# Kernel tuning notes

Hardware: AMD Instinct MI355X
Metric: run time of the kernel (lower is better)

Reference implementation:

```python
import jax, jax.numpy as jnp
import numpy as np

N_NODES = 50000
N_EDGES = 500000
MUL0, MUL1 = 16, 8          # multiplicities of 0e and 1o irreps (in == out)
DIM = MUL0 + 3 * MUL1       # 40
N_BASIS, MID = 10, 32
WNUM = MUL0*MUL0 + MUL1*MUL0 + MUL0*MUL1 + MUL1*MUL1  # 576
INV_SQRT3 = 1.0 / np.sqrt(3.0)  # wigner-3j normalization for l=1 paths
FAN_IN = MUL0 + MUL1        # paths into each output irrep: 16 + 8 = 24
A0 = np.sqrt(1.0 / FAN_IN)  # sqrt((2*0+1)/fan_in)
A1 = np.sqrt(3.0 / FAN_IN)  # sqrt((2*1+1)/fan_in)
LN_EPS = 1e-5


def setup_inputs() -> dict:
    key = jax.random.key(0)
    ks = jax.random.split(key, 8)
    return {
        "x": jax.random.normal(ks[0], (N_NODES, DIM), jnp.float32),
        "edge_sh": jax.random.normal(ks[1], (N_EDGES, 4), jnp.float32),
        "edge_length_embedded": jax.random.uniform(ks[2], (N_EDGES, N_BASIS), jnp.float32),
        "W1": jax.random.normal(ks[3], (N_BASIS, MID), jnp.float32),
        "W2": jax.random.normal(ks[4], (MID, WNUM), jnp.float32),
        "gamma": jnp.ones((DIM,), jnp.float32),
        "beta": jnp.zeros((DIM,), jnp.float32),
        "edge_src": jax.random.randint(ks[5], (N_EDGES,), 0, N_NODES),
        "edge_dst": jax.random.randint(ks[6], (N_EDGES,), 0, N_NODES),
        "avg_num_neighbors": 10,
    }


def reference(x, edge_sh, edge_length_embedded, W1, W2, gamma, beta,
              edge_src, edge_dst, avg_num_neighbors):
    # radial MLP -> per-edge tensor-product weights (e3nn FullyConnectedNet style)
    h = jax.nn.silu(edge_length_embedded @ W1 / jnp.sqrt(jnp.float32(N_BASIS)))
    w = h @ W2 / jnp.sqrt(jnp.float32(MID))              # [E, 576]

    # gather node features onto edges and split into irrep blocks
    xg = x[edge_src]                                     # [E, 40]
    s = xg[:, :MUL0]                                     # [E, 16]  scalars 0e
    v = xg[:, MUL0:].reshape(-1, MUL1, 3)                # [E, 8, 3] vectors 1o
    sh0 = edge_sh[:, 0]                                  # [E]
    sh1 = edge_sh[:, 1:4]                                # [E, 3]

    # split per-edge weights by tensor-product path
    o0, o1, o2 = MUL0*MUL0, MUL0*MUL0 + MUL1*MUL0, MUL0*MUL0 + MUL1*MUL0 + MUL0*MUL1
    W_ss0 = w[:, :o0].reshape(-1, MUL0, MUL0)            # 0e x 0e -> 0e
    W_vv0 = w[:, o0:o1].reshape(-1, MUL1, MUL0)          # 1o x 1o -> 0e
    W_sv1 = w[:, o1:o2].reshape(-1, MUL0, MUL1)          # 0e x 1o -> 1o
    W_vs1 = w[:, o2:].reshape(-1, MUL1, MUL1)            # 1o x 0e -> 1o

    # weighted Clebsch-Gordan tensor product (per edge)
    vdot = jnp.einsum('eui,ei->eu', v, sh1) * INV_SQRT3  # CG 1x1->0
    out0 = A0 * (jnp.einsum('euk,eu->ek', W_ss0, s * sh0[:, None])
                 + jnp.einsum('euk,eu->ek', W_vv0, vdot))            # [E, 16]
    out1 = A1 * INV_SQRT3 * (
        jnp.einsum('euk,eu->ek', W_sv1, s)[:, :, None] * sh1[:, None, :]
        + jnp.einsum('euk,eui->eki', W_vs1, v) * sh0[:, None, None])  # [E, 8, 3]
    edge_values = jnp.concatenate([out0, out1.reshape(-1, 3 * MUL1)], axis=1)

    # scatter-sum into destination nodes, degree normalization, layernorm
    node = jax.ops.segment_sum(edge_values, edge_dst, num_segments=N_NODES)
    node = node / jnp.sqrt(jnp.float32(avg_num_neighbors))
    mu = node.mean(axis=-1, keepdims=True)
    var = node.var(axis=-1, keepdims=True)
    return (node - mu) * jax.lax.rsqrt(var + LN_EPS) * gamma + beta
```

## Files before the change

kernel.cpp:

```cpp
#include <hip/hip_runtime.h>
#include <hip/hip_bf16.h>

#define N_NODES 50000
#define N_EDGES 500000
#define MUL0 16
#define MUL1 8
#define DIM 40
#define N_BASIS 10
#define MID 32
#define WNUM 576
#define SCAN_BLOCKS 196
#define N_GROUPS (N_EDGES / 16)

typedef __attribute__((ext_vector_type(8))) short bf16x8_t;
typedef __attribute__((ext_vector_type(4))) float f32x4_t;

__device__ __forceinline__ float bf2f(unsigned short u) {
  return __uint_as_float(((unsigned int)u) << 16);
}
__device__ __forceinline__ unsigned short f2bf(float f) {
  unsigned int x = __float_as_uint(f);
  unsigned int r = x + 0x7fffu + ((x >> 16) & 1u);
  return (unsigned short)(r >> 16);
}
__device__ __forceinline__ unsigned pk2bf(float a, float b) {
  float2 f; f.x = a; f.y = b;
  __hip_bfloat162 h = __float22bfloat162_rn(f);
  return *reinterpret_cast<unsigned*>(&h);
}
__device__ __forceinline__ bool detect_bf16(const void* gamma) {
  return ((const unsigned int*)gamma)[0] == 0x3F803F80u;
}
template <bool BF16>
__device__ __forceinline__ float ld(const void* p, size_t i) {
  if (BF16) return bf2f(((const unsigned short*)p)[i]);
  return ((const float*)p)[i];
}

#define C_INV_SQRT10 0.31622776601683794f
#define C_INV_SQRT32 0.17677669529663687f
#define C_INV_SQRT3  0.5773502691896258f
#define C_A0C        0.20412414523193154f

__device__ __forceinline__ f32x4_t mfma16x16x32(bf16x8_t a, bf16x8_t b, f32x4_t c) {
  return __builtin_amdgcn_mfma_f32_16x16x32_bf16(a, b, c, 0, 0, 0);
}

__device__ __forceinline__ void gload4(const float* g, float* l) {
  __builtin_amdgcn_global_load_lds(
      (const __attribute__((address_space(1))) void*)g,
      (__attribute__((address_space(3))) void*)l, 4, 0, 0);
}

__global__ __launch_bounds__(256) void rank_kernel(
    const int* __restrict__ edge_dst, int* __restrict__ cnt,
    int* __restrict__ rank) {
  int e = blockIdx.x * 256 + threadIdx.x;
  if (e < N_EDGES) rank[e] = atomicAdd(&cnt[edge_dst[e]], 1);
}

__global__ __launch_bounds__(256) void scanA_kernel(
    const int* __restrict__ cnt, int* __restrict__ off, int* __restrict__ btot) {
  __shared__ int s[256];
  const int tid = threadIdx.x;
  const int i = blockIdx.x * 256 + tid;
  int v = (i < N_NODES) ? cnt[i] : 0;
  s[tid] = v;
  __syncthreads();
  for (int d = 1; d < 256; d <<= 1) {
    int t = (tid >= d) ? s[tid - d] : 0;
    __syncthreads();
    s[tid] += t;
    __syncthreads();
  }
  if (i < N_NODES) off[i] = s[tid] - v;
  if (tid == 255) btot[blockIdx.x] = s[255];
}

__global__ __launch_bounds__(256) void scanB_kernel(
    const int* __restrict__ btot, int* __restrict__ off) {
  __shared__ int s[256];
  __shared__ int basev;
  const int tid = threadIdx.x;
  int v = (tid < SCAN_BLOCKS) ? btot[tid] : 0;
  s[tid] = v;
  __syncthreads();
  for (int d = 1; d < 256; d <<= 1) {
    int t = (tid >= d) ? s[tid - d] : 0;
    __syncthreads();
    s[tid] += t;
    __syncthreads();
  }
  if (tid == 0) basev = (blockIdx.x == 0) ? 0 : s[blockIdx.x - 1];
  __syncthreads();
  const int i = blockIdx.x * 256 + tid;
  if (i < N_NODES) off[i] += basev;
}


#define STAGE_OPS 11

__device__ __forceinline__ void stage_issue(float* Sn, int g, int psrc,
                                            const float* xf, const float* shf,
                                            int lane) {
  const int quad = lane >> 4;
  const int l16  = lane & 15;
  gload4(shf + ((size_t)g * 16 + l16) * 4 + quad, Sn);
  const float* gx = xf + (size_t)psrc * DIM + quad;
  #pragma unroll
  for (int i = 0; i < 10; ++i) {
    float* lb = (i < 4) ? (Sn + 64 + 64 * i) : (Sn + 192 + 64 * i);
    gload4(gx + i * 4, lb);
  }
}

template <bool BF16>
__device__ void edge_mfma_body(
    const void* __restrict__ x,
    const void* __restrict__ edge_sh,
    const void* __restrict__ elemb,
    const void* __restrict__ W1,
    const void* __restrict__ W2,
    const int* __restrict__ edge_src,
    const int* __restrict__ edge_dst,
    const int* __restrict__ rank,
    const int* __restrict__ off,
    unsigned short* __restrict__ ev,
    short* __restrict__ w2b, float* __restrict__ w1s, float* __restrict__ stg)
{
  const int tid = threadIdx.x;

  for (int i = tid; i < 36 * 512; i += 256) {
    int m = i / WNUM;
    int col = i - m * WNUM;
    int q = m >> 3, j = m & 7;
    int t = col >> 4, n = col & 15;
    short val;
    if (BF16) val = (short)((const unsigned short*)W2)[i];
    else      val = (short)f2bf(((const float*)W2)[i]);
    w2b[t * 512 + q * 128 + n * 8 + j] = val;
  }
  for (int i = tid; i < N_BASIS * MID; i += 256) w1s[i] = ld<BF16>(W1, i);
  __syncthreads();

  const int lane = tid & 63;
  const int wid  = tid >> 6;
  const int quad = lane >> 4;
  const int l16  = lane & 15;
  float* Sw = stg + wid * 1664;

  if constexpr (BF16) {
    float* S = Sw;
    for (int gi = blockIdx.x * 4 + wid; gi < N_GROUPS; gi += gridDim.x * 4) {
      const int e0 = gi * 16;
      __builtin_amdgcn_wave_barrier();
      const int eL   = e0 + l16;
      const int dL   = edge_dst[eL];
      const int posv = off[dL] + rank[eL];
      const int posA = __shfl(posv, lane >> 2, 64);
      const int posB = posv;
      if (lane < 16) {
        uint2 sw = *reinterpret_cast<const uint2*>(
            (const unsigned short*)edge_sh + (size_t)(e0 + lane) * 4);
        S[0 * 16 + lane] = __uint_as_float(sw.x << 16);
        S[1 * 16 + lane] = __uint_as_float(sw.x & 0xffff0000u);
        S[2 * 16 + lane] = __uint_as_float(sw.y << 16);
        S[3 * 16 + lane] = __uint_as_float(sw.y & 0xffff0000u);
      }
      {
        const int src = edge_src[e0 + l16];
        const uint4* xr = reinterpret_cast<const uint4*>(
            (const unsigned short*)x + (size_t)src * DIM);
        uint4 c = xr[quad];
        unsigned wv[4] = {c.x, c.y, c.z, c.w};
        #pragma unroll
        for (int p = 0; p < 4; ++p) {
          int col = quad * 8 + 2 * p;
          float lo = __uint_as_float(wv[p] << 16);
          float hi = __uint_as_float(wv[p] & 0xffff0000u);
          int off0 = (col < 16) ? (64 + col * 16) : (448 + (col - 16) * 16);
          int off1 = (col + 1 < 16) ? (64 + (col + 1) * 16) : (448 + (col - 15) * 16);
          S[off0 + l16] = lo;
          S[off1 + l16] = hi;
        }
        if (lane < 16) {
          uint4 c4 = xr[4];
          unsigned wv4[4] = {c4.x, c4.y, c4.z, c4.w};
          #pragma unroll
          for (int p = 0; p < 4; ++p) {
            int col = 32 + 2 * p;
            S[448 + (col - 16) * 16 + lane] = __uint_as_float(wv4[p] << 16);
            S[448 + (col - 15) * 16 + lane] = __uint_as_float(wv4[p] & 0xffff0000u);
          }
        }
      }
      __builtin_amdgcn_wave_barrier();
      #pragma unroll
      for (int p = 0; p < 2; ++p) {
        int idx = lane + p * 64;
        int u = idx >> 4, e = idx & 15;
        float vdv = (S[448 + (u * 3 + 0) * 16 + e] * S[16 + e] +
                     S[448 + (u * 3 + 1) * 16 + e] * S[32 + e] +
                     S[448 + (u * 3 + 2) * 16 + e] * S[48 + e]) * C_INV_SQRT3;
        S[320 + u * 16 + e] = vdv;
      }
      __builtin_amdgcn_wave_barrier();
      bf16x8_t af;
      {
        float eb[N_BASIS];
        const unsigned short* er = (const unsigned short*)elemb + (size_t)(e0 + l16) * N_BASIS;
        #pragma unroll
        for (int p = 0; p < 5; ++p) {
          unsigned uv = *reinterpret_cast<const unsigned*>(er + p * 2);
          eb[2 * p]     = __uint_as_float(uv << 16);
          eb[2 * p + 1] = __uint_as_float(uv & 0xffff0000u);
        }
        float hv[8];
        #pragma unroll
        for (int j = 0; j < 8; ++j) {
          int k = quad * 8 + j;
          float p = 0.f;
          #pragma unroll
          for (int b = 0; b < N_BASIS; ++b) p += eb[b] * w1s[b * MID + k];
          float z = p * C_INV_SQRT10;
          hv[j] = z / (1.f + __expf(-z)) * C_INV_SQRT32;
        }
        __align__(16) unsigned au[4];
        #pragma unroll
        for (int j = 0; j < 4; ++j) au[j] = pk2bf(hv[2 * j], hv[2 * j + 1]);
        af = *reinterpret_cast<const bf16x8_t*>(au);
      }
      f32x4_t s0 = *reinterpret_cast<const f32x4_t*>(&S[quad * 4]);
      f32x4_t out0 = {0.f,0.f,0.f,0.f}, tsv = {0.f,0.f,0.f,0.f};
      f32x4_t tv0 = {0.f,0.f,0.f,0.f}, tv1 = {0.f,0.f,0.f,0.f}, tv2 = {0.f,0.f,0.f,0.f};
      const f32x4_t zero = {0.f,0.f,0.f,0.f};
      const int usel = (l16 >> 3);
      #pragma unroll
      for (int t = 0; t < 16; ++t) {
        bf16x8_t bf = *reinterpret_cast<const bf16x8_t*>(&w2b[t * 512 + lane * 8]);
        f32x4_t D = mfma16x16x32(af, bf, zero);
        f32x4_t sv = *reinterpret_cast<const f32x4_t*>(&S[64 + t * 16 + quad * 4]);
        out0 += D * (sv * s0);
      }
      #pragma unroll
      for (int t = 0; t < 8; ++t) {
        bf16x8_t bf = *reinterpret_cast<const bf16x8_t*>(&w2b[(16 + t) * 512 + lane * 8]);
        f32x4_t D = mfma16x16x32(af, bf, zero);
        f32x4_t vdv = *reinterpret_cast<const f32x4_t*>(&S[320 + t * 16 + quad * 4]);
        out0 += D * vdv;
      }
      #pragma unroll
      for (int t = 0; t < 8; ++t) {
        bf16x8_t bf = *reinterpret_cast<const bf16x8_t*>(&w2b[(24 + t) * 512 + lane * 8]);
        f32x4_t D = mfma16x16x32(af, bf, zero);
        int u = 2 * t + usel;
        f32x4_t sv = *reinterpret_cast<const f32x4_t*>(&S[64 + u * 16 + quad * 4]);
        tsv += D * sv;
      }
      #pragma unroll
      for (int t = 0; t < 4; ++t) {
        bf16x8_t bf = *reinterpret_cast<const bf16x8_t*>(&w2b[(32 + t) * 512 + lane * 8]);
        f32x4_t D = mfma16x16x32(af, bf, zero);
        int u = 2 * t + usel;
        f32x4_t v0 = *reinterpret_cast<const f32x4_t*>(&S[448 + (u * 3 + 0) * 16 + quad * 4]);
        f32x4_t v1 = *reinterpret_cast<const f32x4_t*>(&S[448 + (u * 3 + 1) * 16 + quad * 4]);
        f32x4_t v2 = *reinterpret_cast<const f32x4_t*>(&S[448 + (u * 3 + 2) * 16 + quad * 4]);
        tv0 += D * v0; tv1 += D * v1; tv2 += D * v2;
      }
      #pragma unroll
      for (int r = 0; r < 4; ++r) {
        tsv[r] += __shfl_xor(tsv[r], 8, 64);
        tv0[r] += __shfl_xor(tv0[r], 8, 64);
        tv1[r] += __shfl_xor(tv1[r], 8, 64);
        tv2[r] += __shfl_xor(tv2[r], 8, 64);
      }
      __builtin_amdgcn_wave_barrier();
      #pragma unroll
      for (int r = 0; r < 4; ++r)
        S[64 + (quad * 4 + r) * 42 + l16] = C_A0C * out0[r];
      if (l16 < 8) {
        f32x4_t h1x = *reinterpret_cast<const f32x4_t*>(&S[16 + quad * 4]);
        f32x4_t h1y = *reinterpret_cast<const f32x4_t*>(&S[32 + quad * 4]);
        f32x4_t h1z = *reinterpret_cast<const f32x4_t*>(&S[48 + quad * 4]);
        #pragma unroll
        for (int r = 0; r < 4; ++r) {
          int rowb = 64 + (quad * 4 + r) * 42 + 16 + 3 * l16;
          S[rowb + 0] = C_A0C * (tsv[r] * h1x[r] + tv0[r] * s0[r]);
          S[rowb + 1] = C_A0C * (tsv[r] * h1y[r] + tv1[r] * s0[r]);
          S[rowb + 2] = C_A0C * (tsv[r] * h1z[r] + tv2[r] * s0[r]);
        }
      }
      __builtin_amdgcn_wave_barrier();
      {
        const int edge = lane >> 2, chunk = lane & 3;
        const float* rp = &S[64 + edge * 42 + chunk * 8];
        uint4 t;
        t.x = pk2bf(rp[0], rp[1]); t.y = pk2bf(rp[2], rp[3]);
        t.z = pk2bf(rp[4], rp[5]); t.w = pk2bf(rp[6], rp[7]);
        *reinterpret_cast<uint4*>(ev + (size_t)posA * DIM + chunk * 8) = t;
        if (lane < 16) {
          const float* rq = &S[64 + lane * 42 + 32];
          uint4 t2;
          t2.x = pk2bf(rq[0], rq[1]); t2.y = pk2bf(rq[2], rq[3]);
          t2.z = pk2bf(rq[4], rq[5]); t2.w = pk2bf(rq[6], rq[7]);
          *reinterpret_cast<uint4*>(ev + (size_t)posB * DIM + 32) = t2;
        }
      }
    }
    return;
  }

  const float* xf  = (const float*)x;
  const float* shf = (const float*)edge_sh;
  const int stride = gridDim.x * 4;
  const int gi0 = blockIdx.x * 4 + wid;

  int pdst, psrc, prank;
  int cdst, crank;
  {
    const int e = gi0 * 16 + l16;
    pdst = edge_dst[e]; psrc = edge_src[e]; prank = rank[e];
  }
  stage_issue(Sw, gi0, psrc, xf, shf, lane);
  cdst = pdst; crank = prank;
  {
    const int g1 = gi0 + stride;
    if (g1 < N_GROUPS) {
      const int e = g1 * 16 + l16;
      pdst = edge_dst[e]; psrc = edge_src[e]; prank = rank[e];
    }
  }

  int cur = 0;
  for (int gi = gi0; gi < N_GROUPS; gi += stride, cur ^= 1) {
    float* S  = Sw + cur * 832;
    float* Sn = Sw + (cur ^ 1) * 832;
    const int e0 = gi * 16;
    const int g1 = gi + stride;

    __builtin_amdgcn_wave_barrier();
    if (g1 < N_GROUPS) {
      stage_issue(Sn, g1, psrc, xf, shf, lane);
      asm volatile("s_waitcnt vmcnt(11)" ::: "memory");
    } else {
      asm volatile("s_waitcnt vmcnt(0)" ::: "memory");
    }
    __builtin_amdgcn_sched_barrier(0);

    const int ndst = pdst, nrank = prank;
    {
      const int g2 = g1 + stride;
      if (g2 < N_GROUPS) {
        const int e = g2 * 16 + l16;
        pdst = edge_dst[e]; psrc = edge_src[e]; prank = rank[e];
      }
    }
    const int posv = off[cdst] + crank;
    const int posA = __shfl(posv, lane >> 2, 64);
    const int posB = posv;

    #pragma unroll
    for (int p = 0; p < 2; ++p) {
      int idx = lane + p * 64;
      int u = idx >> 4, e = idx & 15;
      float vdv = (S[448 + (u * 3 + 0) * 16 + e] * S[16 + e] +
                   S[448 + (u * 3 + 1) * 16 + e] * S[32 + e] +
                   S[448 + (u * 3 + 2) * 16 + e] * S[48 + e]) * C_INV_SQRT3;
      S[320 + u * 16 + e] = vdv;
    }
    __builtin_amdgcn_wave_barrier();

    bf16x8_t af;
    {
      float eb[N_BASIS];
      const float* er = (const float*)elemb + (size_t)(e0 + l16) * N_BASIS;
      #pragma unroll
      for (int p = 0; p < 5; ++p) {
        float2 fv = *reinterpret_cast<const float2*>(er + p * 2);
        eb[2 * p] = fv.x; eb[2 * p + 1] = fv.y;
      }
      float hv[8];
      #pragma unroll
      for (int j = 0; j < 8; ++j) {
        int k = quad * 8 + j;
        float p = 0.f;
        #pragma unroll
        for (int b = 0; b < N_BASIS; ++b) p += eb[b] * w1s[b * MID + k];
        float z = p * C_INV_SQRT10;
        hv[j] = z / (1.f + __expf(-z)) * C_INV_SQRT32;
      }
      __align__(16) unsigned au[4];
      #pragma unroll
      for (int j = 0; j < 4; ++j) au[j] = pk2bf(hv[2 * j], hv[2 * j + 1]);
      af = *reinterpret_cast<const bf16x8_t*>(au);
    }

    f32x4_t s0 = *reinterpret_cast<const f32x4_t*>(&S[quad * 4]);

    f32x4_t out0 = {0.f, 0.f, 0.f, 0.f};
    f32x4_t tsv  = {0.f, 0.f, 0.f, 0.f};
    f32x4_t tv0  = {0.f, 0.f, 0.f, 0.f};
    f32x4_t tv1  = {0.f, 0.f, 0.f, 0.f};
    f32x4_t tv2  = {0.f, 0.f, 0.f, 0.f};
    const f32x4_t zero = {0.f, 0.f, 0.f, 0.f};
    const int usel = (l16 >> 3);

    #pragma unroll
    for (int t = 0; t < 16; ++t) {
      bf16x8_t bf = *reinterpret_cast<const bf16x8_t*>(&w2b[t * 512 + lane * 8]);
      f32x4_t D = mfma16x16x32(af, bf, zero);
      f32x4_t sv = *reinterpret_cast<const f32x4_t*>(&S[64 + t * 16 + quad * 4]);
      out0 += D * (sv * s0);
    }
    #pragma unroll
    for (int t = 0; t < 8; ++t) {
      bf16x8_t bf = *reinterpret_cast<const bf16x8_t*>(&w2b[(16 + t) * 512 + lane * 8]);
      f32x4_t D = mfma16x16x32(af, bf, zero);
      f32x4_t vdv = *reinterpret_cast<const f32x4_t*>(&S[320 + t * 16 + quad * 4]);
      out0 += D * vdv;
    }
    #pragma unroll
    for (int t = 0; t < 8; ++t) {
      bf16x8_t bf = *reinterpret_cast<const bf16x8_t*>(&w2b[(24 + t) * 512 + lane * 8]);
      f32x4_t D = mfma16x16x32(af, bf, zero);
      int u = 2 * t + usel;
      f32x4_t sv = *reinterpret_cast<const f32x4_t*>(&S[64 + u * 16 + quad * 4]);
      tsv += D * sv;
    }
    #pragma unroll
    for (int t = 0; t < 4; ++t) {
      bf16x8_t bf = *reinterpret_cast<const bf16x8_t*>(&w2b[(32 + t) * 512 + lane * 8]);
      f32x4_t D = mfma16x16x32(af, bf, zero);
      int u = 2 * t + usel;
      f32x4_t v0 = *reinterpret_cast<const f32x4_t*>(&S[448 + (u * 3 + 0) * 16 + quad * 4]);
      f32x4_t v1 = *reinterpret_cast<const f32x4_t*>(&S[448 + (u * 3 + 1) * 16 + quad * 4]);
      f32x4_t v2 = *reinterpret_cast<const f32x4_t*>(&S[448 + (u * 3 + 2) * 16 + quad * 4]);
      tv0 += D * v0; tv1 += D * v1; tv2 += D * v2;
    }

    #pragma unroll
    for (int r = 0; r < 4; ++r) {
      tsv[r] += __shfl_xor(tsv[r], 8, 64);
      tv0[r] += __shfl_xor(tv0[r], 8, 64);
      tv1[r] += __shfl_xor(tv1[r], 8, 64);
      tv2[r] += __shfl_xor(tv2[r], 8, 64);
    }
    __builtin_amdgcn_wave_barrier();

    #pragma unroll
    for (int r = 0; r < 4; ++r)
      S[64 + (quad * 4 + r) * 42 + l16] = C_A0C * out0[r];
    if (l16 < 8) {
      f32x4_t h1x = *reinterpret_cast<const f32x4_t*>(&S[16 + quad * 4]);
      f32x4_t h1y = *reinterpret_cast<const f32x4_t*>(&S[32 + quad * 4]);
      f32x4_t h1z = *reinterpret_cast<const f32x4_t*>(&S[48 + quad * 4]);
      #pragma unroll
      for (int r = 0; r < 4; ++r) {
        int rowb = 64 + (quad * 4 + r) * 42 + 16 + 3 * l16;
        S[rowb + 0] = C_A0C * (tsv[r] * h1x[r] + tv0[r] * s0[r]);
        S[rowb + 1] = C_A0C * (tsv[r] * h1y[r] + tv1[r] * s0[r]);
        S[rowb + 2] = C_A0C * (tsv[r] * h1z[r] + tv2[r] * s0[r]);
      }
    }
    __builtin_amdgcn_wave_barrier();

    {
      const int edge = lane >> 2, chunk = lane & 3;
      const float* rp = &S[64 + edge * 42 + chunk * 8];
      uint4 t;
      t.x = pk2bf(rp[0], rp[1]); t.y = pk2bf(rp[2], rp[3]);
      t.z = pk2bf(rp[4], rp[5]); t.w = pk2bf(rp[6], rp[7]);
      *reinterpret_cast<uint4*>(ev + (size_t)posA * DIM + chunk * 8) = t;
      if (lane < 16) {
        const float* rq = &S[64 + lane * 42 + 32];
        uint4 t2;
        t2.x = pk2bf(rq[0], rq[1]); t2.y = pk2bf(rq[2], rq[3]);
        t2.z = pk2bf(rq[4], rq[5]); t2.w = pk2bf(rq[6], rq[7]);
        *reinterpret_cast<uint4*>(ev + (size_t)posB * DIM + 32) = t2;
      }
    }

    cdst = ndst; crank = nrank;
  }
}

__global__ __launch_bounds__(256, 2) void edge_mfma_kernel(
    const void* __restrict__ x,
    const void* __restrict__ edge_sh,
    const void* __restrict__ elemb,
    const void* __restrict__ W1,
    const void* __restrict__ W2,
    const void* __restrict__ gamma,
    const int* __restrict__ edge_src,
    const int* __restrict__ edge_dst,
    const int* __restrict__ rank,
    const int* __restrict__ off,
    unsigned short* __restrict__ ev)
{
  __shared__ __align__(16) short w2b[36 * 512];
  __shared__ __align__(16) float w1s[N_BASIS * MID];
  __shared__ __align__(16) float stg[4 * 1664];

  if (detect_bf16(gamma))
    edge_mfma_body<true >(x, edge_sh, elemb, W1, W2, edge_src, edge_dst, rank,
                          off, ev, w2b, w1s, stg);
  else
    edge_mfma_body<false>(x, edge_sh, elemb, W1, W2, edge_src, edge_dst, rank,
                          off, ev, w2b, w1s, stg);
}


#define NPW 12

template <bool BF16>
__device__ __forceinline__ void node_body(
    const unsigned short* __restrict__ ev,
    const int* __restrict__ cnt,
    const int* __restrict__ off,
    const void* __restrict__ gamma,
    const void* __restrict__ beta,
    const int* __restrict__ avg,
    void* __restrict__ out, int lane, int wv)
{
  const int slot = lane / 5;
  const int q    = lane - slot * 5;
  const int base = lane - q;
  const int n    = wv * NPW + slot;
  const bool valid = (slot < NPW) && (n < N_NODES);

  float s[8];
  #pragma unroll
  for (int d = 0; d < 8; ++d) s[d] = 0.f;

  int c = 0, o = 0;
  if (valid) { c = cnt[n]; o = off[n]; }

  const uint4* p = reinterpret_cast<const uint4*>(ev) + (size_t)o * 5 + q;
  int j = 0;
  for (; j + 1 < c; j += 2) {
    uint4 w0 = p[(size_t)j * 5];
    uint4 w1 = p[(size_t)(j + 1) * 5];
    unsigned a0[4] = {w0.x, w0.y, w0.z, w0.w};
    unsigned a1[4] = {w1.x, w1.y, w1.z, w1.w};
    #pragma unroll
    for (int k = 0; k < 4; ++k) {
      s[2 * k + 0] += __uint_as_float(a0[k] << 16) + __uint_as_float(a1[k] << 16);
      s[2 * k + 1] += __uint_as_float(a0[k] & 0xffff0000u) +
                      __uint_as_float(a1[k] & 0xffff0000u);
    }
  }
  if (j < c) {
    uint4 w0 = p[(size_t)j * 5];
    unsigned a0[4] = {w0.x, w0.y, w0.z, w0.w};
    #pragma unroll
    for (int k = 0; k < 4; ++k) {
      s[2 * k + 0] += __uint_as_float(a0[k] << 16);
      s[2 * k + 1] += __uint_as_float(a0[k] & 0xffff0000u);
    }
  }

  const float inv = rsqrtf((float)avg[0]);
  float psum = 0.f;
  #pragma unroll
  for (int d = 0; d < 8; ++d) { s[d] *= inv; psum += s[d]; }
  float m = 0.f;
  #pragma unroll
  for (int i = 0; i < 5; ++i) m += __shfl(psum, base + i, 64);
  const float mean = m * (1.f / DIM);
  float pvar = 0.f;
  #pragma unroll
  for (int d = 0; d < 8; ++d) { float dd = s[d] - mean; pvar += dd * dd; }
  float vv = 0.f;
  #pragma unroll
  for (int i = 0; i < 5; ++i) vv += __shfl(pvar, base + i, 64);
  const float var = vv * (1.f / DIM);
  const float r = rsqrtf(var + 1e-5f);

  if (!valid) return;
  const int gb = q * 8;
  if (BF16) {
    const uint4 g4 = reinterpret_cast<const uint4*>(gamma)[q];
    const uint4 b4 = reinterpret_cast<const uint4*>(beta)[q];
    unsigned gw[4] = {g4.x, g4.y, g4.z, g4.w};
    unsigned bw[4] = {b4.x, b4.y, b4.z, b4.w};
    uint4 t;
    unsigned tw[4];
    #pragma unroll
    for (int k = 0; k < 4; ++k) {
      float y0 = (s[2*k+0] - mean) * r * __uint_as_float(gw[k] << 16) +
                 __uint_as_float(bw[k] << 16);
      float y1 = (s[2*k+1] - mean) * r * __uint_as_float(gw[k] & 0xffff0000u) +
                 __uint_as_float(bw[k] & 0xffff0000u);
      tw[k] = pk2bf(y0, y1);
    }
    t.x = tw[0]; t.y = tw[1]; t.z = tw[2]; t.w = tw[3];
    *reinterpret_cast<uint4*>((unsigned short*)out + (size_t)n * DIM + gb) = t;
  } else {
    const float4 g0 = reinterpret_cast<const float4*>(gamma)[q * 2];
    const float4 g1 = reinterpret_cast<const float4*>(gamma)[q * 2 + 1];
    const float4 b0 = reinterpret_cast<const float4*>(beta)[q * 2];
    const float4 b1 = reinterpret_cast<const float4*>(beta)[q * 2 + 1];
    float4* op = reinterpret_cast<float4*>((float*)out + (size_t)n * DIM + gb);
    float4 t0, t1;
    t0.x = (s[0] - mean) * r * g0.x + b0.x;
    t0.y = (s[1] - mean) * r * g0.y + b0.y;
    t0.z = (s[2] - mean) * r * g0.z + b0.z;
    t0.w = (s[3] - mean) * r * g0.w + b0.w;
    t1.x = (s[4] - mean) * r * g1.x + b1.x;
    t1.y = (s[5] - mean) * r * g1.y + b1.y;
    t1.z = (s[6] - mean) * r * g1.z + b1.z;
    t1.w = (s[7] - mean) * r * g1.w + b1.w;
    op[0] = t0; op[1] = t1;
  }
}

__global__ __launch_bounds__(256) void node_kernel(
    const unsigned short* __restrict__ ev,
    const int* __restrict__ cnt,
    const int* __restrict__ off,
    const void* __restrict__ gamma,
    const void* __restrict__ beta,
    const int* __restrict__ avg,
    void* __restrict__ out)
{
  const int lane = threadIdx.x & 63;
  const int wv = blockIdx.x * 4 + (threadIdx.x >> 6);
  if (detect_bf16(gamma)) node_body<true >(ev, cnt, off, gamma, beta, avg, out, lane, wv);
  else                    node_body<false>(ev, cnt, off, gamma, beta, avg, out, lane, wv);
}

extern "C" void kernel_launch(void* const* d_in, const int* in_sizes, int n_in,
                              void* d_out, int out_size, void* d_ws, size_t ws_size,
                              hipStream_t stream) {
  const void* x       = d_in[0];
  const void* edge_sh = d_in[1];
  const void* elemb   = d_in[2];
  const void* W1      = d_in[3];
  const void* W2      = d_in[4];
  const void* gamma   = d_in[5];
  const void* beta    = d_in[6];
  const int* edge_src = (const int*)d_in[7];
  const int* edge_dst = (const int*)d_in[8];
  const int* avg      = (const int*)d_in[9];

  char* wsb = (char*)d_ws;
  unsigned short* ev = (unsigned short*)(wsb);
  int* rank  = (int*)(wsb + 40000000);
  int* cnt   = (int*)(wsb + 42000000);
  int* off   = (int*)(wsb + 42200000);
  int* btot  = (int*)(wsb + 42400000);

  hipMemsetAsync(cnt, 0, 200000, stream);

  const int EB = (N_EDGES + 255) / 256;
  rank_kernel <<<EB, 256, 0, stream>>>(edge_dst, cnt, rank);
  scanA_kernel<<<SCAN_BLOCKS, 256, 0, stream>>>(cnt, off, btot);
  scanB_kernel<<<SCAN_BLOCKS, 256, 0, stream>>>(btot, off);

  edge_mfma_kernel<<<512, 256, 0, stream>>>(x, edge_sh, elemb, W1, W2, gamma,
                                            edge_src, edge_dst, rank, off, ev);

  node_kernel<<<(N_NODES + 4 * NPW - 1) / (4 * NPW), 256, 0, stream>>>(
      ev, cnt, off, gamma, beta, avg, d_out);
}
```

Measured before the change: 209.8 us.

## Keep W2 MFMA B-fragments in registers instead of LDS, vectorize radial MLP

Each lane now loads its 36 bf16x8 W2 fragments directly from global memory into registers once per block. The 36 KB LDS staging copy of W2 is removed, along with the per-iteration LDS reads that fed the MFMAs. The first radial MLP layer is also restructured to use vector LDS reads of W1 rows with accumulate-over-basis. This adds 144 VGPRs per lane, which risks spilling or lower occupancy under the launch bound of 2 blocks. The vmcnt wait threshold is adjusted to match the changed number of outstanding loads.

```diff
diff --git a/kernel.cpp b/kernel.cpp
--- a/kernel.cpp
+++ b/kernel.cpp
@@ -98,8 +98,6 @@
 }
 
 
-#define STAGE_OPS 11
-
 __device__ __forceinline__ void stage_issue(float* Sn, int g, int psrc,
                                             const float* xf, const float* shf,
                                             int lane) {
@@ -111,6 +109,38 @@
   for (int i = 0; i < 10; ++i) {
     float* lb = (i < 4) ? (Sn + 64 + 64 * i) : (Sn + 192 + 64 * i);
     gload4(gx + i * 4, lb);
+  }
+}
+
+template <bool BF16>
+__device__ __forceinline__ void load_wb(const void* W2, int quad, int l16,
+                                        bf16x8_t* wb) {
+  if constexpr (BF16) {
+    const unsigned short* wcol = (const unsigned short*)W2 +
+                                 (size_t)(quad * 8) * WNUM + l16;
+    #pragma unroll
+    for (int t = 0; t < 36; ++t) {
+      __align__(16) unsigned au[4];
+      #pragma unroll
+      for (int jp = 0; jp < 4; ++jp) {
+        unsigned lo = wcol[(size_t)(2 * jp) * WNUM + 16 * t];
+        unsigned hi = wcol[(size_t)(2 * jp + 1) * WNUM + 16 * t];
+        au[jp] = lo | (hi << 16);
+      }
+      wb[t] = *reinterpret_cast<const bf16x8_t*>(au);
+    }
+  } else {
+    const float* wcol = (const float*)W2 + (size_t)(quad * 8) * WNUM + l16;
+    #pragma unroll
+    for (int t = 0; t < 36; ++t) {
+      __align__(16) unsigned au[4];
+      #pragma unroll
+      for (int jp = 0; jp < 4; ++jp) {
+        au[jp] = pk2bf(wcol[(size_t)(2 * jp) * WNUM + 16 * t],
+                       wcol[(size_t)(2 * jp + 1) * WNUM + 16 * t]);
+      }
+      wb[t] = *reinterpret_cast<const bf16x8_t*>(au);
+    }
   }
 }
 
@@ -126,28 +156,20 @@
     const int* __restrict__ rank,
     const int* __restrict__ off,
     unsigned short* __restrict__ ev,
-    short* __restrict__ w2b, float* __restrict__ w1s, float* __restrict__ stg)
+    float* __restrict__ w1s, float* __restrict__ stg)
 {
   const int tid = threadIdx.x;
-
-  for (int i = tid; i < 36 * 512; i += 256) {
-    int m = i / WNUM;
-    int col = i - m * WNUM;
-    int q = m >> 3, j = m & 7;
-    int t = col >> 4, n = col & 15;
-    short val;
-    if (BF16) val = (short)((const unsigned short*)W2)[i];
-    else      val = (short)f2bf(((const float*)W2)[i]);
-    w2b[t * 512 + q * 128 + n * 8 + j] = val;
-  }
   for (int i = tid; i < N_BASIS * MID; i += 256) w1s[i] = ld<BF16>(W1, i);
-  __syncthreads();
 
   const int lane = tid & 63;
   const int wid  = tid >> 6;
   const int quad = lane >> 4;
   const int l16  = lane & 15;
   float* Sw = stg + wid * 1664;
+
+  bf16x8_t wb[36];
+  load_wb<BF16>(W2, quad, l16, wb);
+  __syncthreads();
 
   if constexpr (BF16) {
     float* S = Sw;
@@ -217,12 +239,18 @@
         }
         float hv[8];
         #pragma unroll
+        for (int j = 0; j < 8; ++j) hv[j] = 0.f;
+        #pragma unroll
+        for (int b = 0; b < N_BASIS; ++b) {
+          const float e = eb[b];
+          f32x4_t wA = *reinterpret_cast<const f32x4_t*>(&w1s[b * MID + quad * 8]);
+          f32x4_t wB = *reinterpret_cast<const f32x4_t*>(&w1s[b * MID + quad * 8 + 4]);
+          hv[0] += e * wA[0]; hv[1] += e * wA[1]; hv[2] += e * wA[2]; hv[3] += e * wA[3];
+          hv[4] += e * wB[0]; hv[5] += e * wB[1]; hv[6] += e * wB[2]; hv[7] += e * wB[3];
+        }
+        #pragma unroll
         for (int j = 0; j < 8; ++j) {
-          int k = quad * 8 + j;
-          float p = 0.f;
-          #pragma unroll
-          for (int b = 0; b < N_BASIS; ++b) p += eb[b] * w1s[b * MID + k];
-          float z = p * C_INV_SQRT10;
+          float z = hv[j] * C_INV_SQRT10;
           hv[j] = z / (1.f + __expf(-z)) * C_INV_SQRT32;
         }
         __align__(16) unsigned au[4];
@@ -237,30 +265,26 @@
       const int usel = (l16 >> 3);
       #pragma unroll
       for (int t = 0; t < 16; ++t) {
-        bf16x8_t bf = *reinterpret_cast<const bf16x8_t*>(&w2b[t * 512 + lane * 8]);
-        f32x4_t D = mfma16x16x32(af, bf, zero);
+        f32x4_t D = mfma16x16x32(af, wb[t], zero);
         f32x4_t sv = *reinterpret_cast<const f32x4_t*>(&S[64 + t * 16 + quad * 4]);
         out0 += D * (sv * s0);
       }
       #pragma unroll
       for (int t = 0; t < 8; ++t) {
-        bf16x8_t bf = *reinterpret_cast<const bf16x8_t*>(&w2b[(16 + t) * 512 + lane * 8]);
-        f32x4_t D = mfma16x16x32(af, bf, zero);
+        f32x4_t D = mfma16x16x32(af, wb[16 + t], zero);
         f32x4_t vdv = *reinterpret_cast<const f32x4_t*>(&S[320 + t * 16 + quad * 4]);
         out0 += D * vdv;
       }
       #pragma unroll
       for (int t = 0; t < 8; ++t) {
-        bf16x8_t bf = *reinterpret_cast<const bf16x8_t*>(&w2b[(24 + t) * 512 + lane * 8]);
-        f32x4_t D = mfma16x16x32(af, bf, zero);
+        f32x4_t D = mfma16x16x32(af, wb[24 + t], zero);
         int u = 2 * t + usel;
         f32x4_t sv = *reinterpret_cast<const f32x4_t*>(&S[64 + u * 16 + quad * 4]);
         tsv += D * sv;
       }
       #pragma unroll
       for (int t = 0; t < 4; ++t) {
-        bf16x8_t bf = *reinterpret_cast<const bf16x8_t*>(&w2b[(32 + t) * 512 + lane * 8]);
-        f32x4_t D = mfma16x16x32(af, bf, zero);
+        f32x4_t D = mfma16x16x32(af, wb[32 + t], zero);
         int u = 2 * t + usel;
         f32x4_t v0 = *reinterpret_cast<const f32x4_t*>(&S[448 + (u * 3 + 0) * 16 + quad * 4]);
         f32x4_t v1 = *reinterpret_cast<const f32x4_t*>(&S[448 + (u * 3 + 1) * 16 + quad * 4]);
@@ -341,7 +365,7 @@
     __builtin_amdgcn_wave_barrier();
     if (g1 < N_GROUPS) {
       stage_issue(Sn, g1, psrc, xf, shf, lane);
-      asm volatile("s_waitcnt vmcnt(11)" ::: "memory");
+      asm volatile("s_waitcnt vmcnt(16)" ::: "memory");
     } else {
       asm volatile("s_waitcnt vmcnt(0)" ::: "memory");
     }
@@ -381,12 +405,18 @@
       }
       float hv[8];
       #pragma unroll
+      for (int j = 0; j < 8; ++j) hv[j] = 0.f;
+      #pragma unroll
+      for (int b = 0; b < N_BASIS; ++b) {
+        const float e = eb[b];
+        f32x4_t wA = *reinterpret_cast<const f32x4_t*>(&w1s[b * MID + quad * 8]);
+        f32x4_t wB = *reinterpret_cast<const f32x4_t*>(&w1s[b * MID + quad * 8 + 4]);
+        hv[0] += e * wA[0]; hv[1] += e * wA[1]; hv[2] += e * wA[2]; hv[3] += e * wA[3];
+        hv[4] += e * wB[0]; hv[5] += e * wB[1]; hv[6] += e * wB[2]; hv[7] += e * wB[3];
+      }
+      #pragma unroll
       for (int j = 0; j < 8; ++j) {
-        int k = quad * 8 + j;
-        float p = 0.f;
-        #pragma unroll
-        for (int b = 0; b < N_BASIS; ++b) p += eb[b] * w1s[b * MID + k];
-        float z = p * C_INV_SQRT10;
+        float z = hv[j] * C_INV_SQRT10;
         hv[j] = z / (1.f + __expf(-z)) * C_INV_SQRT32;
       }
       __align__(16) unsigned au[4];
@@ -407,30 +437,26 @@
 
     #pragma unroll
     for (int t = 0; t < 16; ++t) {
-      bf16x8_t bf = *reinterpret_cast<const bf16x8_t*>(&w2b[t * 512 + lane * 8]);
-      f32x4_t D = mfma16x16x32(af, bf, zero);
+      f32x4_t D = mfma16x16x32(af, wb[t], zero);
       f32x4_t sv = *reinterpret_cast<const f32x4_t*>(&S[64 + t * 16 + quad * 4]);
       out0 += D * (sv * s0);
     }
     #pragma unroll
     for (int t = 0; t < 8; ++t) {
-      bf16x8_t bf = *reinterpret_cast<const bf16x8_t*>(&w2b[(16 + t) * 512 + lane * 8]);
-      f32x4_t D = mfma16x16x32(af, bf, zero);
+      f32x4_t D = mfma16x16x32(af, wb[16 + t], zero);
       f32x4_t vdv = *reinterpret_cast<const f32x4_t*>(&S[320 + t * 16 + quad * 4]);
       out0 += D * vdv;
     }
     #pragma unroll
     for (int t = 0; t < 8; ++t) {
-      bf16x8_t bf = *reinterpret_cast<const bf16x8_t*>(&w2b[(24 + t) * 512 + lane * 8]);
-      f32x4_t D = mfma16x16x32(af, bf, zero);
+      f32x4_t D = mfma16x16x32(af, wb[24 + t], zero);
       int u = 2 * t + usel;
       f32x4_t sv = *reinterpret_cast<const f32x4_t*>(&S[64 + u * 16 + quad * 4]);
       tsv += D * sv;
     }
     #pragma unroll
     for (int t = 0; t < 4; ++t) {
-      bf16x8_t bf = *reinterpret_cast<const bf16x8_t*>(&w2b[(32 + t) * 512 + lane * 8]);
-      f32x4_t D = mfma16x16x32(af, bf, zero);
+      f32x4_t D = mfma16x16x32(af, wb[32 + t], zero);
       int u = 2 * t + usel;
       f32x4_t v0 = *reinterpret_cast<const f32x4_t*>(&S[448 + (u * 3 + 0) * 16 + quad * 4]);
       f32x4_t v1 = *reinterpret_cast<const f32x4_t*>(&S[448 + (u * 3 + 1) * 16 + quad * 4]);
@@ -497,16 +523,15 @@
     const int* __restrict__ off,
     unsigned short* __restrict__ ev)
 {
-  __shared__ __align__(16) short w2b[36 * 512];
   __shared__ __align__(16) float w1s[N_BASIS * MID];
   __shared__ __align__(16) float stg[4 * 1664];
 
   if (detect_bf16(gamma))
     edge_mfma_body<true >(x, edge_sh, elemb, W1, W2, edge_src, edge_dst, rank,
-                          off, ev, w2b, w1s, stg);
+                          off, ev, w1s, stg);
   else
     edge_mfma_body<false>(x, edge_sh, elemb, W1, W2, edge_src, edge_dst, rank,
-                          off, ev, w2b, w1s, stg);
+                          off, ev, w1s, stg);
 }
 
 
```

Result: slower. 240.5 us (+14.6%).
